# Kernel optimization log

Measured on AMD Instinct MI355X. Metric: run time of the kernel, lower is better.

The kernel has to match this reference:

```python
import jax, jax.numpy as jnp
import numpy as np

QW_MAX = 127  # 2**(8-1) - 1


def setup_inputs() -> dict:
    key = jax.random.key(0)
    k1, k2, k3, k4, k5 = jax.random.split(key, 5)
    B, Din, H, Dout = 4096, 1024, 4096, 1024
    x = jax.random.normal(k1, (B, Din), dtype=jnp.float32)
    # float master weights (already transposed, as in quantify_weights: weight.T)
    w1f = jax.random.normal(k2, (Din, H), dtype=jnp.float32) * 0.02
    b1f = jax.random.normal(k3, (H,), dtype=jnp.float32) * 0.02
    w2f = jax.random.normal(k4, (H, Dout), dtype=jnp.float32) * 0.02
    b2f = jax.random.normal(k5, (Dout,), dtype=jnp.float32) * 0.02
    return {"x": x, "w1f": w1f, "b1f": b1f, "w2f": w2f, "b2f": b2f}


def _quantify_pair(w, b):
    # joint max-abs scale over weight and bias (matches quantify(x, x2))
    max_v = jnp.maximum(jnp.max(jnp.abs(w)), jnp.max(jnp.abs(b)))
    scale = max_v / QW_MAX
    wq = jnp.round(w / scale).astype(jnp.int8)
    bq = jnp.round(b / scale).astype(jnp.int8)
    return wq, bq, scale


def _dot_product(q_a, q_b, scale_a, scale_b, target_scale):
    # int8 GEMM with int32 accumulation, then requantize to int16
    y0 = q_a.astype(jnp.int32) @ q_b.astype(jnp.int32)  # [M, N] int32
    scale = scale_a * scale_b / target_scale
    return jnp.round(y0 * scale).astype(jnp.int16)


def reference(x, w1f, b1f, w2f, b2f):
    # weight quantization (done once at init in torch, inlined here)
    w1, b1, s1 = _quantify_pair(w1f, b1f)
    w2, b2, s2 = _quantify_pair(w2f, b2f)
    # dynamic activation quantization
    x_scale = jnp.max(jnp.abs(x)) / QW_MAX
    x_q = jnp.round(x / x_scale).astype(jnp.int8)
    # layer 1: target_scale = s1, so effective multiplier is x_scale
    o1 = _dot_product(x_q, w1, x_scale, s1, s1) + b1.astype(jnp.int16)
    # layer 2: note torch passes scale_1 (not x_scale) here — faithful to source
    o2 = _dot_product(jnp.maximum(o1, 0), w2, s1, s2, s2) + b2.astype(jnp.int16)
    # dequantize
    return o2.astype(jnp.float32) * s2
```

## Files before the change

### kernel.cpp

```cpp
#include <hip/hip_runtime.h>
#include <stdint.h>

typedef int   i32x4 __attribute__((ext_vector_type(4)));
typedef float f32x4 __attribute__((ext_vector_type(4)));

#define WS_PART    0
#define WS_XQ      32768
#define WS_W1QT    (WS_XQ   + 4096*1024)
#define WS_W2QT    (WS_W1QT + 4096*1024)
#define WS_PS      (WS_W2QT + 4096*1024)
#define WS_PH      (WS_PS   + 4096*4096)

__device__ __forceinline__ void async16(const void* g, void* l) {
  __builtin_amdgcn_global_load_lds(
      (const __attribute__((address_space(1))) unsigned*)g,
      (__attribute__((address_space(3))) unsigned*)l, 16, 0, 0);
}

__device__ __forceinline__ float block_absmax(const float* __restrict__ p0, int n0,
                                              const float* __restrict__ p1, int n1,
                                              float* red, float* slot) {
  int tid = threadIdx.x, nt = blockDim.x;
  float m = 0.f;
  for (int i = tid; i < n0; i += nt) m = fmaxf(m, fabsf(p0[i]));
  if (p1) for (int i = tid; i < n1; i += nt) m = fmaxf(m, fabsf(p1[i]));
  for (int off = 32; off; off >>= 1) m = fmaxf(m, __shfl_down(m, off));
  if ((tid & 63) == 0) red[tid >> 6] = m;
  __syncthreads();
  if (tid == 0) {
    int nw = nt >> 6;
    float M = red[0];
    for (int w = 1; w < nw; w++) M = fmaxf(M, red[w]);
    *slot = M;
  }
  __syncthreads();
  return *slot;
}

__global__ void k_absmax3(const float* __restrict__ x, const float* __restrict__ w1,
                          const float* __restrict__ w2, float* __restrict__ part) {
  int seg = blockIdx.x >> 9;
  int b = blockIdx.x & 511;
  const float* p = (seg == 0) ? x : (seg == 1) ? w1 : w2;
  int i = b * 256 + threadIdx.x;
  float m = 0.f;
  #pragma unroll
  for (int it = 0; it < 8; it++) {
    f32x4 v = ((const f32x4*)p)[i + it * 131072];
    m = fmaxf(m, fmaxf(fmaxf(fabsf(v.x), fabsf(v.y)), fmaxf(fabsf(v.z), fabsf(v.w))));
  }
  for (int off = 32; off; off >>= 1) m = fmaxf(m, __shfl_down(m, off));
  __shared__ float red[4];
  if ((threadIdx.x & 63) == 0) red[threadIdx.x >> 6] = m;
  __syncthreads();
  if (threadIdx.x == 0)
    part[blockIdx.x] = fmaxf(fmaxf(red[0], red[1]), fmaxf(red[2], red[3]));
}

__device__ __forceinline__ void quantT_body(const float* __restrict__ w, float s,
                                            i32x4* __restrict__ out, int C, int tkbits,
                                            int b) {
  int L = b * 256 + threadIdx.x;
  int h_in = L & 127;
  int kb = (L >> 7) & 3;
  int tk = (L >> 9) & ((1 << tkbits) - 1);
  int hblk = L >> (9 + tkbits);
  int h = hblk * 128 + h_in;
  int k0 = (tk * 4 + kb) * 16;
  int wd[4];
  #pragma unroll
  for (int d = 0; d < 4; d++) {
    unsigned acc = 0;
    #pragma unroll
    for (int j = 0; j < 4; j++) {
      float v = w[(size_t)(k0 + d * 4 + j) * C + h];
      int q = (int)rintf(v / s) & 255;
      acc |= (unsigned)q << (8 * j);
    }
    wd[d] = (int)acc;
  }
  i32x4 o; o.x = wd[0]; o.y = wd[1]; o.z = wd[2]; o.w = wd[3];
  out[L] = o;
}

__global__ void k_prep(const float* __restrict__ x, const float* __restrict__ w1f,
                       const float* __restrict__ w2f, const float* __restrict__ b1f,
                       const float* __restrict__ b2f, const float* __restrict__ part,
                       float* __restrict__ scales,
                       i32x4* __restrict__ xq, i32x4* __restrict__ w1qt,
                       i32x4* __restrict__ w2qt) {
  __shared__ float red[4];
  __shared__ float slot;
  int seg = blockIdx.x >> 10;
  int b = blockIdx.x & 1023;
  if (seg == 0) {
    float s = block_absmax(part, 512, nullptr, 0, red, &slot) / 127.0f;
    if (b == 0 && threadIdx.x == 0) scales[0] = s;
    int L = b * 256 + threadIdx.x;
    int m_in = L & 127, kb = (L >> 7) & 3, tk = (L >> 9) & 15, mblk = L >> 13;
    int m = mblk * 128 + m_in;
    int k0 = (tk * 4 + kb) * 16;
    const f32x4* px = (const f32x4*)(x + m * 1024 + k0);
    int wd[4];
    #pragma unroll
    for (int d = 0; d < 4; d++) {
      f32x4 v = px[d];
      int b0 = (int)rintf(v.x / s) & 255;
      int b1 = (int)rintf(v.y / s) & 255;
      int b2 = (int)rintf(v.z / s) & 255;
      int b3 = (int)rintf(v.w / s) & 255;
      wd[d] = b0 | (b1 << 8) | (b2 << 16) | (b3 << 24);
    }
    i32x4 o; o.x = wd[0]; o.y = wd[1]; o.z = wd[2]; o.w = wd[3];
    xq[L] = o;
  } else if (seg == 1) {
    float s = block_absmax(part + 512, 512, b1f, 4096, red, &slot) / 127.0f;
    if (b == 0 && threadIdx.x == 0) scales[1] = s;
    quantT_body(w1f, s, w1qt, 4096, 4, b);
  } else {
    float s = block_absmax(part + 1024, 512, b2f, 1024, red, &slot) / 127.0f;
    if (b == 0 && threadIdx.x == 0) scales[2] = s;
    quantT_body(w2f, s, w2qt, 1024, 6, b);
  }
}

__launch_bounds__(64)
__global__ void k_gemm1(const i32x4* __restrict__ Aq, const i32x4* __restrict__ Bq,
                        const float* __restrict__ scales, const float* __restrict__ b1f,
                        unsigned* __restrict__ plane_s, unsigned* __restrict__ plane_h) {
  int lane = threadIdx.x;
  int bb = blockIdx.x;
  int hb = blockIdx.y;
  int wid = blockIdx.z;
  int wm = wid & 1, wn = wid >> 1;
  int g = lane >> 4, l15 = lane & 15;

  const i32x4* gA = Aq + (size_t)hb * 16 * 512;
  const i32x4* gB = Bq + (size_t)bb * 16 * 512;
  int aoff = g * 128 + wm * 64 + l15;
  int boff = g * 128 + wn * 64 + l15;

  float sx  = scales[0];
  float s1v = scales[1];
  float mult1 = sx * s1v / s1v;

  i32x4 acc[4][4];
  #pragma unroll
  for (int r = 0; r < 4; r++)
    #pragma unroll
    for (int c = 0; c < 4; c++) acc[r][c] = (i32x4)(0);

  i32x4 af[4], bf[4];
  #pragma unroll
  for (int r = 0; r < 4; r++) af[r] = gA[aoff + r * 16];
  #pragma unroll
  for (int c = 0; c < 4; c++) bf[c] = gB[boff + c * 16];

  for (int t = 0; t < 15; ++t) {
    i32x4 an[4], bn[4];
    const i32x4* ga = gA + (t + 1) * 512;
    const i32x4* gb = gB + (t + 1) * 512;
    #pragma unroll
    for (int r = 0; r < 4; r++) an[r] = ga[aoff + r * 16];
    #pragma unroll
    for (int c = 0; c < 4; c++) bn[c] = gb[boff + c * 16];
    #pragma unroll
    for (int r = 0; r < 4; r++)
      #pragma unroll
      for (int c = 0; c < 4; c++)
        acc[r][c] = __builtin_amdgcn_mfma_i32_16x16x64_i8(af[r], bf[c], acc[r][c], 0, 0, 0);
    #pragma unroll
    for (int r = 0; r < 4; r++) { af[r] = an[r]; bf[r] = bn[r]; }
  }
  #pragma unroll
  for (int r = 0; r < 4; r++)
    #pragma unroll
    for (int c = 0; c < 4; c++)
      acc[r][c] = __builtin_amdgcn_mfma_i32_16x16x64_i8(af[r], bf[c], acc[r][c], 0, 0, 0);

  int t2base = hb * 2 + wm;
  #pragma unroll
  for (int r = 0; r < 4; r++) {
    int hloc = wm * 64 + r * 16 + 4 * g;
    int bq0 = (int)rintf(b1f[hb * 128 + hloc + 0] / s1v);
    int bq1 = (int)rintf(b1f[hb * 128 + hloc + 1] / s1v);
    int bq2 = (int)rintf(b1f[hb * 128 + hloc + 2] / s1v);
    int bq3 = (int)rintf(b1f[hb * 128 + hloc + 3] / s1v);
    #pragma unroll
    for (int c = 0; c < 4; c++) {
      unsigned lo = 0, hi = 0;
      #pragma unroll
      for (int q = 0; q < 4; q++) {
        int y0 = acc[r][c][q];
        int bqv = (q == 0) ? bq0 : (q == 1) ? bq1 : (q == 2) ? bq2 : bq3;
        int o = (short)((int)rintf((float)y0 * mult1) + bqv);
        int a = o > 0 ? o : 0;
        int s8 = (int)(signed char)(a & 0xFF);
        int h8 = (a >> 8) + (s8 < 0 ? 1 : 0);
        lo |= (unsigned)(s8 & 0xFF) << (8 * q);
        hi |= (unsigned)(h8 & 0xFF) << (8 * q);
      }
      int m_in = wn * 64 + c * 16 + l15;
      unsigned idx = (((unsigned)(bb * 64 + t2base) * 512u + (unsigned)(r * 128 + m_in)) << 2) + g;
      plane_s[idx] = lo;
      plane_h[idx] = hi;
    }
  }
}

__launch_bounds__(512, 4)
__global__ void k_gemm2(const i32x4* __restrict__ Ps, const i32x4* __restrict__ Ph,
                        const i32x4* __restrict__ Bq, const float* __restrict__ scales,
                        const float* __restrict__ b2f, float* __restrict__ out) {
  __shared__ i32x4 st[2048];

  int tid = threadIdx.x;
  int L = blockIdx.x;
  int mb = ((L & 7) << 3) | ((L >> 3) & 7);
  int nb = L >> 6;
  int mblk = mb >> 1, half = mb & 1;
  int wid = tid >> 6, lane = tid & 63;
  int kh = wid >> 2, w2 = wid & 3;
  int wm = w2 & 1, wn = w2 >> 1;
  int g = lane >> 4, l15 = lane & 15;
  int t256 = tid & 255;
  int sbase = kh * 1024;
  int a_idx = (t256 >> 6) * 128 + half * 64 + (t256 & 63);
  int b_idx = g * 128 + wn * 64 + l15;

  {
    int t = kh * 32;
    const i32x4* pS = Ps + ((size_t)(mblk * 64 + t) << 9);
    const i32x4* pH = Ph + ((size_t)(mblk * 64 + t) << 9);
    async16(pS + a_idx, &st[sbase + t256]);
    async16(pH + a_idx, &st[sbase + 256 + t256]);
  }
  i32x4 bf[4];
  {
    const i32x4* pB = Bq + ((size_t)(nb * 64 + kh * 32) << 9);
    #pragma unroll
    for (int c = 0; c < 4; c++) bf[c] = pB[b_idx + c * 16];
  }

  float s1v = scales[1];
  float s2v = scales[2];
  float mult2 = s1v * s2v / s2v;
  int bq[4];
  #pragma unroll
  for (int c = 0; c < 4; c++)
    bq[c] = (int)rintf(b2f[nb * 128 + wn * 64 + c * 16 + l15] / s2v);

  i32x4 accS[2][4], accH[2][4];
  #pragma unroll
  for (int r = 0; r < 2; r++)
    #pragma unroll
    for (int c = 0; c < 4; c++) { accS[r][c] = (i32x4)(0); accH[r][c] = (i32x4)(0); }

  __syncthreads();

  for (int tt = 0; tt < 32; ++tt) {
    int cur = tt & 1;
    if (tt + 1 < 32) {
      int t = kh * 32 + tt + 1;
      const i32x4* pS = Ps + ((size_t)(mblk * 64 + t) << 9);
      const i32x4* pH = Ph + ((size_t)(mblk * 64 + t) << 9);
      int R1 = sbase + (cur ^ 1) * 512;
      async16(pS + a_idx, &st[R1 + t256]);
      async16(pH + a_idx, &st[R1 + 256 + t256]);
      __builtin_amdgcn_sched_barrier(0);
    }
    int R = sbase + cur * 512;
    i32x4 aS[2], aH[2];
    #pragma unroll
    for (int r = 0; r < 2; r++) {
      aS[r] = st[R + g * 64 + wm * 32 + r * 16 + l15];
      aH[r] = st[R + 256 + g * 64 + wm * 32 + r * 16 + l15];
    }
    #pragma unroll
    for (int r = 0; r < 2; r++)
      #pragma unroll
      for (int c = 0; c < 4; c++) {
        accS[r][c] = __builtin_amdgcn_mfma_i32_16x16x64_i8(aS[r], bf[c], accS[r][c], 0, 0, 0);
        accH[r][c] = __builtin_amdgcn_mfma_i32_16x16x64_i8(aH[r], bf[c], accH[r][c], 0, 0, 0);
      }
    if (tt + 1 < 32) {
      __builtin_amdgcn_sched_barrier(0);
      const i32x4* pB = Bq + ((size_t)(nb * 64 + kh * 32 + tt + 1) << 9);
      #pragma unroll
      for (int c = 0; c < 4; c++) bf[c] = pB[b_idx + c * 16];
      asm volatile("s_waitcnt vmcnt(4)" ::: "memory");
      __builtin_amdgcn_s_barrier();
      __builtin_amdgcn_sched_barrier(0);
    }
  }

  int y0p[2][4][4];
  #pragma unroll
  for (int r = 0; r < 2; r++)
    #pragma unroll
    for (int c = 0; c < 4; c++)
      #pragma unroll
      for (int q = 0; q < 4; q++)
        y0p[r][c][q] = accS[r][c][q] + accH[r][c][q] * 256;

  __syncthreads();
  int* mg = (int*)st;
  if (kh == 1) {
    #pragma unroll
    for (int r = 0; r < 2; r++)
      #pragma unroll
      for (int c = 0; c < 4; c++)
        #pragma unroll
        for (int q = 0; q < 4; q++)
          mg[((r * 4 + c) * 4 + q) * 256 + t256] = y0p[r][c][q];
  }
  __syncthreads();
  if (kh == 0) {
    #pragma unroll
    for (int r = 0; r < 2; r++) {
      int m0 = mb * 64 + wm * 32 + r * 16 + 4 * g;
      #pragma unroll
      for (int c = 0; c < 4; c++) {
        int n = nb * 128 + wn * 64 + c * 16 + l15;
        #pragma unroll
        for (int q = 0; q < 4; q++) {
          int y0 = y0p[r][c][q] + mg[((r * 4 + c) * 4 + q) * 256 + t256];
          int o = (short)((int)rintf((float)y0 * mult2) + bq[c]);
          out[(size_t)(m0 + q) * 1024 + n] = (float)o * s2v;
        }
      }
    }
  }
}

extern "C" void kernel_launch(void* const* d_in, const int* in_sizes, int n_in,
                              void* d_out, int out_size, void* d_ws, size_t ws_size,
                              hipStream_t stream) {
  const float* x   = (const float*)d_in[0];
  const float* w1f = (const float*)d_in[1];
  const float* b1f = (const float*)d_in[2];
  const float* w2f = (const float*)d_in[3];
  const float* b2f = (const float*)d_in[4];
  float* out = (float*)d_out;

  char* ws = (char*)d_ws;
  float*  part    = (float*)(ws + WS_PART);
  float*  scales  = part + 1536;
  i32x4*  xq      = (i32x4*)(ws + WS_XQ);
  i32x4*  w1qt    = (i32x4*)(ws + WS_W1QT);
  i32x4*  w2qt    = (i32x4*)(ws + WS_W2QT);
  unsigned* ps    = (unsigned*)(ws + WS_PS);
  unsigned* ph    = (unsigned*)(ws + WS_PH);

  k_absmax3<<<1536, 256, 0, stream>>>(x, w1f, w2f, part);
  k_prep<<<3072, 256, 0, stream>>>(x, w1f, w2f, b1f, b2f, part, scales, xq, w1qt, w2qt);
  k_gemm1<<<dim3(32, 32, 4), 64, 0, stream>>>(w1qt, xq, scales, b1f, ps, ph);
  k_gemm2<<<512, 512, 0, stream>>>((const i32x4*)ps, (const i32x4*)ph, w2qt,
                                   scales, b2f, out);
}
```

Baseline: 174.6 us.

## Restructure gemm1 into 512-thread blocks with LDS-staged A, split-K and reduction

The first int8 GEMM moves from 4096 single-wave blocks that each load A and B straight from global memory to 2048 blocks of eight waves. Each block stages a shared A tile in LDS with async global-to-LDS loads and double buffering, and splits K across two wave groups whose partial accumulators are summed through LDS before the requantize epilogue. The block index is remapped so neighbouring blocks share tiles in cache. This aims to cut redundant global loads and improve occupancy and latency hiding, at the cost of barriers, LDS traffic and an extra reduction step.

New measurement: 180.8 us. 1.04x slower.

```diff
diff --git a/kernel.cpp b/kernel.cpp
--- a/kernel.cpp
+++ b/kernel.cpp
@@ -124,86 +124,118 @@
   }
 }
 
-__launch_bounds__(64)
+__launch_bounds__(512, 4)
 __global__ void k_gemm1(const i32x4* __restrict__ Aq, const i32x4* __restrict__ Bq,
                         const float* __restrict__ scales, const float* __restrict__ b1f,
                         unsigned* __restrict__ plane_s, unsigned* __restrict__ plane_h) {
-  int lane = threadIdx.x;
-  int bb = blockIdx.x;
-  int hb = blockIdx.y;
-  int wid = blockIdx.z;
-  int wm = wid & 1, wn = wid >> 1;
+  __shared__ i32x4 st[2048];
+
+  int tid = threadIdx.x;
+  int L = blockIdx.x;
+  int wg = (L & 7) * 256 + (L >> 3);
+  int T  = wg & 63;
+  int bb = wg >> 6;
+  int half = T & 1, hblk = T >> 1;
+  int wid = tid >> 6, lane = tid & 63;
+  int kh = wid >> 2, w2 = wid & 3;
+  int wm = w2 & 1, wn = w2 >> 1;
   int g = lane >> 4, l15 = lane & 15;
-
-  const i32x4* gA = Aq + (size_t)hb * 16 * 512;
-  const i32x4* gB = Bq + (size_t)bb * 16 * 512;
-  int aoff = g * 128 + wm * 64 + l15;
-  int boff = g * 128 + wn * 64 + l15;
+  int t256 = tid & 255;
+  int sbase = kh * 512;
+  int a_src = (t256 >> 6) * 128 + half * 64 + (t256 & 63);
+  int b_idx = g * 128 + wn * 64 + l15;
+
+  const i32x4* gA = Aq + (size_t)hblk * 8192;
+  const i32x4* gB = Bq + (size_t)bb * 8192;
+
+  async16(gA + (size_t)(kh * 8) * 512 + a_src, &st[sbase + t256]);
+  i32x4 bf[4];
+  {
+    const i32x4* pB = gB + (size_t)(kh * 8) * 512;
+    #pragma unroll
+    for (int c = 0; c < 4; c++) bf[c] = pB[b_idx + c * 16];
+  }
 
   float sx  = scales[0];
   float s1v = scales[1];
   float mult1 = sx * s1v / s1v;
 
-  i32x4 acc[4][4];
-  #pragma unroll
-  for (int r = 0; r < 4; r++)
+  i32x4 acc[2][4];
+  #pragma unroll
+  for (int r = 0; r < 2; r++)
     #pragma unroll
     for (int c = 0; c < 4; c++) acc[r][c] = (i32x4)(0);
 
-  i32x4 af[4], bf[4];
-  #pragma unroll
-  for (int r = 0; r < 4; r++) af[r] = gA[aoff + r * 16];
-  #pragma unroll
-  for (int c = 0; c < 4; c++) bf[c] = gB[boff + c * 16];
-
-  for (int t = 0; t < 15; ++t) {
-    i32x4 an[4], bn[4];
-    const i32x4* ga = gA + (t + 1) * 512;
-    const i32x4* gb = gB + (t + 1) * 512;
-    #pragma unroll
-    for (int r = 0; r < 4; r++) an[r] = ga[aoff + r * 16];
-    #pragma unroll
-    for (int c = 0; c < 4; c++) bn[c] = gb[boff + c * 16];
-    #pragma unroll
-    for (int r = 0; r < 4; r++)
+  int aoff = g * 64 + wm * 32 + l15;
+
+  __syncthreads();
+
+  for (int tt = 0; tt < 8; ++tt) {
+    int cur = tt & 1;
+    if (tt + 1 < 8) {
+      async16(gA + (size_t)(kh * 8 + tt + 1) * 512 + a_src,
+              &st[sbase + (cur ^ 1) * 256 + t256]);
+      __builtin_amdgcn_sched_barrier(0);
+    }
+    i32x4 af[2];
+    #pragma unroll
+    for (int r = 0; r < 2; r++) af[r] = st[sbase + cur * 256 + aoff + r * 16];
+    #pragma unroll
+    for (int r = 0; r < 2; r++)
       #pragma unroll
       for (int c = 0; c < 4; c++)
         acc[r][c] = __builtin_amdgcn_mfma_i32_16x16x64_i8(af[r], bf[c], acc[r][c], 0, 0, 0);
-    #pragma unroll
-    for (int r = 0; r < 4; r++) { af[r] = an[r]; bf[r] = bn[r]; }
-  }
-  #pragma unroll
-  for (int r = 0; r < 4; r++)
-    #pragma unroll
-    for (int c = 0; c < 4; c++)
-      acc[r][c] = __builtin_amdgcn_mfma_i32_16x16x64_i8(af[r], bf[c], acc[r][c], 0, 0, 0);
-
-  int t2base = hb * 2 + wm;
-  #pragma unroll
-  for (int r = 0; r < 4; r++) {
-    int hloc = wm * 64 + r * 16 + 4 * g;
-    int bq0 = (int)rintf(b1f[hb * 128 + hloc + 0] / s1v);
-    int bq1 = (int)rintf(b1f[hb * 128 + hloc + 1] / s1v);
-    int bq2 = (int)rintf(b1f[hb * 128 + hloc + 2] / s1v);
-    int bq3 = (int)rintf(b1f[hb * 128 + hloc + 3] / s1v);
-    #pragma unroll
-    for (int c = 0; c < 4; c++) {
-      unsigned lo = 0, hi = 0;
-      #pragma unroll
-      for (int q = 0; q < 4; q++) {
-        int y0 = acc[r][c][q];
-        int bqv = (q == 0) ? bq0 : (q == 1) ? bq1 : (q == 2) ? bq2 : bq3;
-        int o = (short)((int)rintf((float)y0 * mult1) + bqv);
-        int a = o > 0 ? o : 0;
-        int s8 = (int)(signed char)(a & 0xFF);
-        int h8 = (a >> 8) + (s8 < 0 ? 1 : 0);
-        lo |= (unsigned)(s8 & 0xFF) << (8 * q);
-        hi |= (unsigned)(h8 & 0xFF) << (8 * q);
+    if (tt + 1 < 8) {
+      __builtin_amdgcn_sched_barrier(0);
+      const i32x4* pB = gB + (size_t)(kh * 8 + tt + 1) * 512;
+      #pragma unroll
+      for (int c = 0; c < 4; c++) bf[c] = pB[b_idx + c * 16];
+      asm volatile("s_waitcnt vmcnt(4)" ::: "memory");
+      __builtin_amdgcn_s_barrier();
+      __builtin_amdgcn_sched_barrier(0);
+    }
+  }
+
+  __syncthreads();
+  int* mg = (int*)st;
+  if (kh == 1) {
+    #pragma unroll
+    for (int r = 0; r < 2; r++)
+      #pragma unroll
+      for (int c = 0; c < 4; c++)
+        #pragma unroll
+        for (int q = 0; q < 4; q++)
+          mg[((r * 4 + c) * 4 + q) * 256 + t256] = acc[r][c][q];
+  }
+  __syncthreads();
+  if (kh == 0) {
+    #pragma unroll
+    for (int r = 0; r < 2; r++) {
+      int rg = wm * 2 + r;
+      int hbase = T * 64 + wm * 32 + r * 16 + 4 * g;
+      int bq0 = (int)rintf(b1f[hbase + 0] / s1v);
+      int bq1 = (int)rintf(b1f[hbase + 1] / s1v);
+      int bq2 = (int)rintf(b1f[hbase + 2] / s1v);
+      int bq3 = (int)rintf(b1f[hbase + 3] / s1v);
+      #pragma unroll
+      for (int c = 0; c < 4; c++) {
+        unsigned lo = 0, hi = 0;
+        #pragma unroll
+        for (int q = 0; q < 4; q++) {
+          int y0 = acc[r][c][q] + mg[((r * 4 + c) * 4 + q) * 256 + t256];
+          int bqv = (q == 0) ? bq0 : (q == 1) ? bq1 : (q == 2) ? bq2 : bq3;
+          int o = (short)((int)rintf((float)y0 * mult1) + bqv);
+          int a = o > 0 ? o : 0;
+          int s8 = (int)(signed char)(a & 0xFF);
+          int h8 = (a >> 8) + (s8 < 0 ? 1 : 0);
+          lo |= (unsigned)(s8 & 0xFF) << (8 * q);
+          hi |= (unsigned)(h8 & 0xFF) << (8 * q);
+        }
+        int m_in = wn * 64 + c * 16 + l15;
+        unsigned idx = (((unsigned)(bb * 64 + T) * 512u + (unsigned)(rg * 128 + m_in)) << 2) + g;
+        plane_s[idx] = lo;
+        plane_h[idx] = hi;
       }
-      int m_in = wn * 64 + c * 16 + l15;
-      unsigned idx = (((unsigned)(bb * 64 + t2base) * 512u + (unsigned)(r * 128 + m_in)) << 2) + g;
-      plane_s[idx] = lo;
-      plane_h[idx] = hi;
     }
   }
 }
@@ -354,7 +386,7 @@
 
   k_absmax3<<<1536, 256, 0, stream>>>(x, w1f, w2f, part);
   k_prep<<<3072, 256, 0, stream>>>(x, w1f, w2f, b1f, b2f, part, scales, xq, w1qt, w2qt);
-  k_gemm1<<<dim3(32, 32, 4), 64, 0, stream>>>(w1qt, xq, scales, b1f, ps, ph);
+  k_gemm1<<<2048, 512, 0, stream>>>(w1qt, xq, scales, b1f, ps, ph);
   k_gemm2<<<512, 512, 0, stream>>>((const i32x4*)ps, (const i32x4*)ph, w2qt,
                                    scales, b2f, out);
 }
```

## Share gemm1 tiles across four waves via LDS with triple-buffered async loads

Applied to the files above, without the earlier changes.

k_gemm1 previously launched four separate 64-thread blocks per output tile, each loading its A/B fragments directly from global memory into registers. It now runs one 256-thread block per tile, with the four waves sharing A/B k-slices staged in LDS. The slices are fetched by a three-stage global_load_lds pipeline with explicit vmcnt waits and barriers. Bias quantization is also computed once per block into shared memory. The aim is to cut redundant global traffic and hide load latency, at the cost of LDS usage, per-step barriers and hand-tuned waitcnt correctness risk.

After: 165.1 us. 5.4% less time.

```diff
diff --git a/kernel.cpp b/kernel.cpp
--- a/kernel.cpp
+++ b/kernel.cpp
@@ -124,25 +124,36 @@
   }
 }
 
-__launch_bounds__(64)
+__launch_bounds__(256)
 __global__ void k_gemm1(const i32x4* __restrict__ Aq, const i32x4* __restrict__ Bq,
                         const float* __restrict__ scales, const float* __restrict__ b1f,
                         unsigned* __restrict__ plane_s, unsigned* __restrict__ plane_h) {
-  int lane = threadIdx.x;
+  __shared__ i32x4 As[3][512];
+  __shared__ i32x4 Bs[3][512];
+  __shared__ int b1s[128];
+  int tid = threadIdx.x;
   int bb = blockIdx.x;
   int hb = blockIdx.y;
-  int wid = blockIdx.z;
+  int lane = tid & 63, wid = tid >> 6;
   int wm = wid & 1, wn = wid >> 1;
   int g = lane >> 4, l15 = lane & 15;
 
   const i32x4* gA = Aq + (size_t)hb * 16 * 512;
   const i32x4* gB = Bq + (size_t)bb * 16 * 512;
-  int aoff = g * 128 + wm * 64 + l15;
-  int boff = g * 128 + wn * 64 + l15;
+
+  #pragma unroll
+  for (int t = 0; t < 2; ++t) {
+    async16(gA + t * 512 + tid, &As[t][tid]);
+    async16(gA + t * 512 + tid + 256, &As[t][tid + 256]);
+    async16(gB + t * 512 + tid, &Bs[t][tid]);
+    async16(gB + t * 512 + tid + 256, &Bs[t][tid + 256]);
+  }
 
   float sx  = scales[0];
   float s1v = scales[1];
   float mult1 = sx * s1v / s1v;
+  for (int i = tid; i < 128; i += 256)
+    b1s[i] = (int)rintf(b1f[hb * 128 + i] / s1v);
 
   i32x4 acc[4][4];
   #pragma unroll
@@ -150,42 +161,47 @@
     #pragma unroll
     for (int c = 0; c < 4; c++) acc[r][c] = (i32x4)(0);
 
-  i32x4 af[4], bf[4];
-  #pragma unroll
-  for (int r = 0; r < 4; r++) af[r] = gA[aoff + r * 16];
-  #pragma unroll
-  for (int c = 0; c < 4; c++) bf[c] = gB[boff + c * 16];
-
-  for (int t = 0; t < 15; ++t) {
-    i32x4 an[4], bn[4];
-    const i32x4* ga = gA + (t + 1) * 512;
-    const i32x4* gb = gB + (t + 1) * 512;
-    #pragma unroll
-    for (int r = 0; r < 4; r++) an[r] = ga[aoff + r * 16];
-    #pragma unroll
-    for (int c = 0; c < 4; c++) bn[c] = gb[boff + c * 16];
+  int abase = g * 128 + wm * 64 + l15;
+  int bbase = g * 128 + wn * 64 + l15;
+
+  __syncthreads();
+
+  int cb = 0;
+  for (int t = 0; t < 16; ++t) {
+    if (t + 2 < 16) {
+      int pb = cb + 2; if (pb >= 3) pb -= 3;
+      const i32x4* ga = gA + (t + 2) * 512;
+      const i32x4* gb = gB + (t + 2) * 512;
+      async16(ga + tid, &As[pb][tid]);
+      async16(ga + tid + 256, &As[pb][tid + 256]);
+      async16(gb + tid, &Bs[pb][tid]);
+      async16(gb + tid + 256, &Bs[pb][tid + 256]);
+      __builtin_amdgcn_sched_barrier(0);
+    }
+    i32x4 af[4], bf[4];
+    #pragma unroll
+    for (int r = 0; r < 4; r++) af[r] = As[cb][abase + r * 16];
+    #pragma unroll
+    for (int c = 0; c < 4; c++) bf[c] = Bs[cb][bbase + c * 16];
     #pragma unroll
     for (int r = 0; r < 4; r++)
       #pragma unroll
       for (int c = 0; c < 4; c++)
         acc[r][c] = __builtin_amdgcn_mfma_i32_16x16x64_i8(af[r], bf[c], acc[r][c], 0, 0, 0);
-    #pragma unroll
-    for (int r = 0; r < 4; r++) { af[r] = an[r]; bf[r] = bn[r]; }
-  }
-  #pragma unroll
-  for (int r = 0; r < 4; r++)
-    #pragma unroll
-    for (int c = 0; c < 4; c++)
-      acc[r][c] = __builtin_amdgcn_mfma_i32_16x16x64_i8(af[r], bf[c], acc[r][c], 0, 0, 0);
+    if (t < 15) {
+      if (t + 2 < 16) asm volatile("s_waitcnt vmcnt(4)" ::: "memory");
+      else            asm volatile("s_waitcnt vmcnt(0)" ::: "memory");
+      __builtin_amdgcn_s_barrier();
+      __builtin_amdgcn_sched_barrier(0);
+    }
+    cb = cb + 1; if (cb >= 3) cb -= 3;
+  }
 
   int t2base = hb * 2 + wm;
   #pragma unroll
   for (int r = 0; r < 4; r++) {
     int hloc = wm * 64 + r * 16 + 4 * g;
-    int bq0 = (int)rintf(b1f[hb * 128 + hloc + 0] / s1v);
-    int bq1 = (int)rintf(b1f[hb * 128 + hloc + 1] / s1v);
-    int bq2 = (int)rintf(b1f[hb * 128 + hloc + 2] / s1v);
-    int bq3 = (int)rintf(b1f[hb * 128 + hloc + 3] / s1v);
+    int bq0 = b1s[hloc], bq1 = b1s[hloc + 1], bq2 = b1s[hloc + 2], bq3 = b1s[hloc + 3];
     #pragma unroll
     for (int c = 0; c < 4; c++) {
       unsigned lo = 0, hi = 0;
@@ -354,7 +370,7 @@
 
   k_absmax3<<<1536, 256, 0, stream>>>(x, w1f, w2f, part);
   k_prep<<<3072, 256, 0, stream>>>(x, w1f, w2f, b1f, b2f, part, scales, xq, w1qt, w2qt);
-  k_gemm1<<<dim3(32, 32, 4), 64, 0, stream>>>(w1qt, xq, scales, b1f, ps, ph);
+  k_gemm1<<<dim3(32, 32), 256, 0, stream>>>(w1qt, xq, scales, b1f, ps, ph);
   k_gemm2<<<512, 512, 0, stream>>>((const i32x4*)ps, (const i32x4*)ph, w2qt,
                                    scales, b2f, out);
 }
```
